# Performance work log

Hardware: AMD Instinct MI355X
Metric: run time of the kernel (lower is better)

Reference implementation:

```python
import jax, jax.numpy as jnp
import numpy as np


def setup_inputs() -> dict:
    key = jax.random.key(0)
    ks = jax.random.split(key, 9)
    B, L, Dh, Din = 8, 2048, 256, 1024  # Dh = hidden_size = input_dim // num_heads
    s = 0.05
    return {
        "x": jax.random.normal(ks[0], (B, L, Dh), dtype=jnp.float32),
        "Wq": jax.random.normal(ks[1], (Dh, Dh), dtype=jnp.float32) * s,
        "bq": jax.random.normal(ks[2], (Dh,), dtype=jnp.float32) * s,
        "Wk": jax.random.normal(ks[3], (Dh, Dh), dtype=jnp.float32) * s,
        "bk": jax.random.normal(ks[4], (Dh,), dtype=jnp.float32) * s,
        "Wv": jax.random.normal(ks[5], (Dh, Dh), dtype=jnp.float32) * s,
        "bv": jax.random.normal(ks[6], (Dh,), dtype=jnp.float32) * s,
        "Wo": jax.random.normal(ks[7], (Dh, Din), dtype=jnp.float32) * s,
        "bo": jax.random.normal(ks[8], (Din,), dtype=jnp.float32) * s,
        "num_heads": 4,
    }


def reference(x, Wq, bq, Wk, bk, Wv, bv, Wo, bo, num_heads):
    B, L, d = x.shape  # d == hidden_size; scale uses this full dim per the source
    H = num_heads
    hd = d // H
    # QKV projections (weights stored [in, out])
    Q = (x @ Wq + bq).reshape(B, L, H, hd).transpose(0, 2, 1, 3)  # [B,H,L,hd]
    K = (x @ Wk + bk).reshape(B, L, H, hd).transpose(0, 2, 1, 3)
    V = (x @ Wv + bv).reshape(B, L, H, hd).transpose(0, 2, 1, 3)
    scale = 1.0 / jnp.sqrt(jnp.float32(d))  # source divides by dim**0.5 with dim = x.shape[-1]
    scores = jnp.einsum("bhqd,bhkd->bhqk", Q, K) * scale  # [B,H,L,L]
    weights = jax.nn.softmax(scores, axis=-1)
    # dropout is identity in eval mode
    ctx = jnp.einsum("bhqk,bhkd->bhqd", weights, V)  # [B,H,L,hd]
    ctx = ctx.transpose(0, 2, 1, 3).reshape(B, L, d)
    return ctx @ Wo + bo  # [B,L,input_dim]
```

## Files before the change

kernel.cpp:

```cpp
#include <hip/hip_runtime.h>

#define SEQ   2048
#define NH    4
#define HD    64
#define DH    256
#define DIN   1024
#define MTOK  16384
#define BH    32

typedef _Float16 half8 __attribute__((ext_vector_type(8)));
typedef _Float16 half4 __attribute__((ext_vector_type(4)));
typedef float    floatx4 __attribute__((ext_vector_type(4)));

__device__ __forceinline__ floatx4 mfma16(half8 a, half8 b, floatx4 c) {
    return __builtin_amdgcn_mfma_f32_16x16x32_f16(a, b, c, 0, 0, 0);
}

#if __has_builtin(__builtin_amdgcn_exp2f)
#define EXP2(x) __builtin_amdgcn_exp2f(x)
#else
#define EXP2(x) exp2f(x)
#endif

__device__ __forceinline__ int swz(int r, int g) {
    return r * 64 + ((g ^ (r & 7)) << 3);
}

__device__ __forceinline__ void glds16(const _Float16* g, _Float16* l) {
    __builtin_amdgcn_global_load_lds(
        (const __attribute__((address_space(1))) void*)g,
        (__attribute__((address_space(3))) void*)l, 16, 0, 0);
}

#define QSCALE 0.09016844005556021f

__global__ __launch_bounds__(256) void cvt_kernel(
    const float* __restrict__ x, const float* __restrict__ Wq,
    const float* __restrict__ Wk, const float* __restrict__ Wv,
    const float* __restrict__ Wo, _Float16* __restrict__ xh,
    _Float16* __restrict__ Wtq, _Float16* __restrict__ WoT)
{
    const int t = threadIdx.x;
    if (blockIdx.x < 2048) {
        const size_t i = ((size_t)blockIdx.x * 256 + t) * 8;
        const float4 f0 = *(const float4*)(x + i);
        const float4 f1 = *(const float4*)(x + i + 4);
        half8 h;
        h[0]=(_Float16)f0.x; h[1]=(_Float16)f0.y; h[2]=(_Float16)f0.z; h[3]=(_Float16)f0.w;
        h[4]=(_Float16)f1.x; h[5]=(_Float16)f1.y; h[6]=(_Float16)f1.z; h[7]=(_Float16)f1.w;
        *(half8*)(xh + i) = h;
        return;
    }
    const int wb = blockIdx.x - 2048;
    const int nb = (wb % 28) * 64;
    const int kb = (wb / 28) * 64;
    const float* src; int ld, nc0;
    _Float16* dstbase; int nrow0;
    if (nb < 768) {
        src = (nb < 256) ? Wq : (nb < 512) ? Wk : Wv;
        ld = DH; nc0 = nb & 255; dstbase = Wtq; nrow0 = nb;
    } else { src = Wo; ld = DIN; nc0 = nb - 768; dstbase = WoT; nrow0 = nb - 768; }

    __shared__ float Ts[64][65];
    const int c = t & 63, r0 = t >> 6;
#pragma unroll
    for (int rr = 0; rr < 16; rr++)
        Ts[r0 + rr * 4][c] = src[(size_t)(kb + r0 + rr * 4) * ld + nc0 + c];
    __syncthreads();
    const int nr = t >> 2, kc = (t & 3) * 16;
    _Float16 hv[16];
#pragma unroll
    for (int j = 0; j < 16; j++) hv[j] = (_Float16)Ts[kc + j][nr];
    *(half8*)&dstbase[(size_t)(nrow0 + nr) * 256 + kb + kc]     = *(half8*)&hv[0];
    *(half8*)&dstbase[(size_t)(nrow0 + nr) * 256 + kb + kc + 8] = *(half8*)&hv[8];
}

__global__ __launch_bounds__(256) void qkv_kernel(
    const _Float16* __restrict__ xh, const _Float16* __restrict__ Wtq,
    const float* __restrict__ bq, const float* __restrict__ bk,
    const float* __restrict__ bv,
    _Float16* __restrict__ Qo, _Float16* __restrict__ Ko, _Float16* __restrict__ Vt)
{
    const int mb = blockIdx.x * 128;
    const int nb = blockIdx.y * 128;
    const int t = threadIdx.x, lane = t & 63, w = t >> 6;
    const int quad = lane >> 4, l16 = lane & 15;
    const int wr = (w >> 1) * 64, wc = (w & 1) * 64;
    const int which = nb >> 8;

    __shared__ _Float16 Ah[128 * 64];
    __shared__ _Float16 Bh[128 * 64];

    floatx4 acc[4][4] = {};

    const int srow = w * 8 + (lane >> 3);
    const int slg  = (lane & 7) ^ ((lane >> 3) & 7);
    const int sbase = w * 64;

    for (int k0 = 0; k0 < DH; k0 += 64) {
        __syncthreads();
#pragma unroll
        for (int c = 0; c < 4; c++) {
            glds16(xh + (size_t)(mb + c * 32 + srow) * DH + k0 + slg * 8,
                   &Ah[(c * 256 + sbase) * 8]);
            glds16(Wtq + (size_t)(nb + c * 32 + srow) * DH + k0 + slg * 8,
                   &Bh[(c * 256 + sbase) * 8]);
        }
        __syncthreads();
#pragma unroll
        for (int kh = 0; kh < 2; kh++) {
            half8 af[4], bf[4];
#pragma unroll
            for (int i = 0; i < 4; i++) {
                af[i] = *(const half8*)&Ah[swz(wr + i * 16 + l16, kh * 4 + quad)];
                bf[i] = *(const half8*)&Bh[swz(wc + i * 16 + l16, kh * 4 + quad)];
            }
            if (which == 2) {
#pragma unroll
                for (int mt = 0; mt < 4; mt++)
#pragma unroll
                    for (int nt = 0; nt < 4; nt++)
                        acc[mt][nt] = mfma16(af[mt], bf[nt], acc[mt][nt]);
            } else {
#pragma unroll
                for (int mt = 0; mt < 4; mt++)
#pragma unroll
                    for (int nt = 0; nt < 4; nt++)
                        acc[mt][nt] = mfma16(bf[nt], af[mt], acc[mt][nt]);
            }
        }
    }

    if (which == 2) {
#pragma unroll
        for (int nt = 0; nt < 4; nt++) {
            const int c2 = (nb & 255) + wc + nt * 16 + l16;
            const float bb = bv[c2];
            const int h = c2 >> 6, hd = c2 & 63;
#pragma unroll
            for (int mt = 0; mt < 4; mt++) {
                const int mr0 = mb + wr + mt * 16 + quad * 4;
                const int b = mr0 >> 11, lt0 = mr0 & (SEQ - 1);
                const int bh = b * NH + h;
                half4 hv;
#pragma unroll
                for (int i = 0; i < 4; i++) hv[i] = (_Float16)(acc[mt][nt][i] + bb);
                *(half4*)&Vt[((size_t)bh * HD + hd) * SEQ + lt0] = hv;
            }
        }
    } else {
        const float* bias = (which == 0) ? bq : bk;
        const float qs = (which == 0) ? QSCALE : 1.0f;
        _Float16* Out = (which == 0) ? Qo : Ko;
#pragma unroll
        for (int nt = 0; nt < 4; nt++) {
            const int c2b = (nb & 255) + wc + nt * 16 + quad * 4;
            const float4 bb4 = *(const float4*)&bias[c2b];
            const int h = c2b >> 6, hd0 = c2b & 63;
#pragma unroll
            for (int mt = 0; mt < 4; mt++) {
                const int tok = mb + wr + mt * 16 + l16;
                const int b = tok >> 11, lt = tok & (SEQ - 1);
                const int bh = b * NH + h;
                half4 hv;
                hv[0] = (_Float16)((acc[mt][nt][0] + bb4.x) * qs);
                hv[1] = (_Float16)((acc[mt][nt][1] + bb4.y) * qs);
                hv[2] = (_Float16)((acc[mt][nt][2] + bb4.z) * qs);
                hv[3] = (_Float16)((acc[mt][nt][3] + bb4.w) * qs);
                *(half4*)&Out[((size_t)bh * SEQ + lt) * HD + hd0] = hv;
            }
        }
    }
}

__global__ __launch_bounds__(256, 4) void attn_kernel(
    const _Float16* __restrict__ Q, const _Float16* __restrict__ K,
    const _Float16* __restrict__ Vt, _Float16* __restrict__ Opart,
    float* __restrict__ Lsum, int kspan)
{
    const int bh = blockIdx.y, qb = blockIdx.x * 128, ks = blockIdx.z;
    const int t = threadIdx.x, lane = t & 63, w = t >> 6;
    const int quad = lane >> 4, l16 = lane & 15;

    __shared__ _Float16 Ksm[64 * 64];
    __shared__ _Float16 Vsm[64 * 64];
    __shared__ _Float16 Psm[4 * 32 * 64];

    const _Float16* Kbh = K + (size_t)bh * SEQ * HD;
    const _Float16* Vbh = Vt + (size_t)bh * HD * SEQ;

    half8 qf[2][2];
#pragma unroll
    for (int qt = 0; qt < 2; qt++) {
        const _Float16* qp = Q + ((size_t)bh * SEQ + qb + w * 32 + qt * 16 + l16) * HD;
        qf[qt][0] = *(const half8*)(qp + quad * 8);
        qf[qt][1] = *(const half8*)(qp + 32 + quad * 8);
    }

    floatx4 oacc[2][4] = {};
    float lsum[2] = {0.f, 0.f};

    const int srow = w * 8 + (lane >> 3);
    const int slg  = (lane & 7) ^ ((lane >> 3) & 7);
    const int sbase = w * 64;
    const int pbase = w * 2048;
    const int kb0 = ks * kspan, kb1 = kb0 + kspan;

    for (int kb = kb0; kb < kb1; kb += 64) {
        __syncthreads();
#pragma unroll
        for (int c = 0; c < 2; c++) {
            glds16(Kbh + (size_t)(kb + c * 32 + srow) * HD + slg * 8,
                   &Ksm[(c * 256 + sbase) * 8]);
            glds16(Vbh + (size_t)(c * 32 + srow) * SEQ + kb + slg * 8,
                   &Vsm[(c * 256 + sbase) * 8]);
        }
        __syncthreads();

#pragma unroll
        for (int kt = 0; kt < 4; kt++) {
            const half8 kf0 = *(const half8*)&Ksm[swz(kt * 16 + l16, quad)];
            const half8 kf1 = *(const half8*)&Ksm[swz(kt * 16 + l16, 4 + quad)];
#pragma unroll
            for (int qt = 0; qt < 2; qt++) {
                floatx4 a = {};
                a = mfma16(kf0, qf[qt][0], a);
                a = mfma16(kf1, qf[qt][1], a);
                const float p0 = EXP2(a[0]), p1 = EXP2(a[1]);
                const float p2 = EXP2(a[2]), p3 = EXP2(a[3]);
                lsum[qt] += (p0 + p1) + (p2 + p3);
                half4 hp;
                hp[0] = (_Float16)p0; hp[1] = (_Float16)p1;
                hp[2] = (_Float16)p2; hp[3] = (_Float16)p3;
                const int g = kt * 2 + (quad >> 1);
                *(half4*)&Psm[pbase + (qt * 16 + l16) * 64 +
                              ((g ^ (l16 & 7)) << 3) + (quad & 1) * 4] = hp;
            }
        }

#pragma unroll
        for (int k2 = 0; k2 < 2; k2++) {
            half8 pf[2];
#pragma unroll
            for (int qt = 0; qt < 2; qt++)
                pf[qt] = *(const half8*)&Psm[pbase + swz(qt * 16 + l16, k2 * 4 + quad)];
#pragma unroll
            for (int nt = 0; nt < 4; nt++) {
                const half8 vf = *(const half8*)&Vsm[swz(nt * 16 + l16, k2 * 4 + quad)];
#pragma unroll
                for (int qt = 0; qt < 2; qt++)
                    oacc[qt][nt] = mfma16(vf, pf[qt], oacc[qt][nt]);
            }
        }
    }

#pragma unroll
    for (int qt = 0; qt < 2; qt++) {
        lsum[qt] += __shfl_xor(lsum[qt], 16, 64);
        lsum[qt] += __shfl_xor(lsum[qt], 32, 64);
        if (quad == 0)
            Lsum[((size_t)(ks * BH + bh)) * SEQ + qb + w * 32 + qt * 16 + l16] = lsum[qt];
    }
    _Float16* op = Opart + (((size_t)(ks * BH + bh)) * SEQ + qb + w * 32) * HD;
#pragma unroll
    for (int qt = 0; qt < 2; qt++)
#pragma unroll
        for (int nt = 0; nt < 4; nt++) {
            half4 hv;
#pragma unroll
            for (int i = 0; i < 4; i++) hv[i] = (_Float16)oacc[qt][nt][i];
            *(half4*)&op[(size_t)(qt * 16 + l16) * HD + nt * 16 + quad * 4] = hv;
        }
}

__global__ __launch_bounds__(256) void reduce_kernel(
    const _Float16* __restrict__ Opart, const float* __restrict__ Lsum,
    _Float16* __restrict__ ctx, int nks)
{
    const size_t i = ((size_t)blockIdx.x * 256 + threadIdx.x) * 8;
    const int ch = (int)(i & 255);
    const int h = ch >> 6, hd = ch & 63;
    const int tok = (int)(i >> 8);
    const int b = tok >> 11, l = tok & (SEQ - 1);
    const int bh = b * NH + h;

    float a[8] = {};
    float lt = 0.f;
    for (int ks = 0; ks < nks; ks++) {
        const size_t row = ((size_t)(ks * BH + bh)) * SEQ + l;
        lt += Lsum[row];
        const half8 v = *(const half8*)(Opart + row * HD + hd);
#pragma unroll
        for (int j = 0; j < 8; j++) a[j] += (float)v[j];
    }
    const float inv = 1.0f / lt;
    half8 o;
#pragma unroll
    for (int j = 0; j < 8; j++) o[j] = (_Float16)(a[j] * inv);
    *(half8*)(ctx + i) = o;
}

__global__ __launch_bounds__(256) void out_kernel(
    const _Float16* __restrict__ ctx, const _Float16* __restrict__ WoT,
    const float* __restrict__ bo, float* __restrict__ out)
{
    const int mb = blockIdx.x * 128;
    const int nb = blockIdx.y * 128;
    const int t = threadIdx.x, lane = t & 63, w = t >> 6;
    const int quad = lane >> 4, l16 = lane & 15;
    const int wr = (w >> 1) * 64, wc = (w & 1) * 64;

    __shared__ _Float16 Ah[128 * 64];
    __shared__ _Float16 Bh[128 * 64];

    floatx4 acc[4][4] = {};

    const int srow = w * 8 + (lane >> 3);
    const int slg  = (lane & 7) ^ ((lane >> 3) & 7);
    const int sbase = w * 64;

    for (int k0 = 0; k0 < DH; k0 += 64) {
        __syncthreads();
#pragma unroll
        for (int c = 0; c < 4; c++) {
            glds16(ctx + (size_t)(mb + c * 32 + srow) * DH + k0 + slg * 8,
                   &Ah[(c * 256 + sbase) * 8]);
            glds16(WoT + (size_t)(nb + c * 32 + srow) * DH + k0 + slg * 8,
                   &Bh[(c * 256 + sbase) * 8]);
        }
        __syncthreads();
#pragma unroll
        for (int kh = 0; kh < 2; kh++) {
            half8 af[4], bf[4];
#pragma unroll
            for (int i = 0; i < 4; i++) {
                af[i] = *(const half8*)&Ah[swz(wr + i * 16 + l16, kh * 4 + quad)];
                bf[i] = *(const half8*)&Bh[swz(wc + i * 16 + l16, kh * 4 + quad)];
            }
#pragma unroll
            for (int mt = 0; mt < 4; mt++)
#pragma unroll
                for (int nt = 0; nt < 4; nt++)
                    acc[mt][nt] = mfma16(bf[nt], af[mt], acc[mt][nt]);
        }
    }

#pragma unroll
    for (int nt = 0; nt < 4; nt++) {
        const int col0 = nb + wc + nt * 16 + quad * 4;
        const float4 bb4 = *(const float4*)&bo[col0];
#pragma unroll
        for (int mt = 0; mt < 4; mt++) {
            const int tok = mb + wr + mt * 16 + l16;
            float4 ov;
            ov.x = acc[mt][nt][0] + bb4.x;
            ov.y = acc[mt][nt][1] + bb4.y;
            ov.z = acc[mt][nt][2] + bb4.z;
            ov.w = acc[mt][nt][3] + bb4.w;
            *(float4*)&out[(size_t)tok * DIN + col0] = ov;
        }
    }
}

extern "C" void kernel_launch(void* const* d_in, const int* in_sizes, int n_in,
                              void* d_out, int out_size, void* d_ws, size_t ws_size,
                              hipStream_t stream) {
    (void)in_sizes; (void)n_in; (void)out_size;
    const float* x  = (const float*)d_in[0];
    const float* Wq = (const float*)d_in[1];
    const float* bq = (const float*)d_in[2];
    const float* Wk = (const float*)d_in[3];
    const float* bk = (const float*)d_in[4];
    const float* Wv = (const float*)d_in[5];
    const float* bv = (const float*)d_in[6];
    const float* Wo = (const float*)d_in[7];
    const float* bo = (const float*)d_in[8];

    const size_t H = (size_t)BH * SEQ * HD;
    _Float16* Qw  = (_Float16*)d_ws;
    _Float16* Kw  = Qw + H;
    _Float16* Vt  = Kw + H;
    _Float16* WoT = Vt + H;
    const size_t lsum_off = 3 * H + 262144;

    const size_t need4 = lsum_off * 2 + (size_t)4 * 65536 * 4 + (size_t)4 * H * 2;
    const int KS = (ws_size >= need4) ? 4 : 2;

    float* Lsum = (float*)(Qw + lsum_off);
    _Float16* Opart = Qw + lsum_off + (size_t)KS * 131072;
    _Float16* xh  = Opart;
    _Float16* Wtq = Opart + (size_t)MTOK * DH;
    _Float16* ctx = Qw;

    cvt_kernel<<<dim3(2048 + 112), 256, 0, stream>>>(x, Wq, Wk, Wv, Wo, xh, Wtq, WoT);
    qkv_kernel<<<dim3(MTOK / 128, 768 / 128), 256, 0, stream>>>(
        xh, Wtq, bq, bk, bv, Qw, Kw, Vt);
    attn_kernel<<<dim3(SEQ / 128, BH, KS), 256, 0, stream>>>(
        Qw, Kw, Vt, Opart, Lsum, SEQ / KS);
    reduce_kernel<<<dim3(MTOK * DH / (256 * 8)), 256, 0, stream>>>(
        Opart, Lsum, ctx, KS);
    out_kernel<<<dim3(MTOK / 128, DIN / 128), 256, 0, stream>>>(
        ctx, WoT, bo, (float*)d_out);
}
```

Measured before the change: 194.7 us.

## Load K/V fragments directly from global into registers, drop LDS staging in attention

The attention kernel stops staging K and V tiles through shared memory with barriers. Each wave now loads its MFMA fragments for K and V straight from global memory into registers, relying on L2/cache reuse across waves. The workspace is reorganised, the key-split count drops from 4/2 to 2/1, and occupancy is lowered to 3 blocks per CU. This removes the barriers and LDS traffic, but each of the four waves now issues its own redundant global loads for the same K/V data, and there are fewer key splits available for parallelism.

```diff
diff --git a/kernel.cpp b/kernel.cpp
--- a/kernel.cpp
+++ b/kernel.cpp
@@ -38,7 +38,7 @@
     const float* __restrict__ x, const float* __restrict__ Wq,
     const float* __restrict__ Wk, const float* __restrict__ Wv,
     const float* __restrict__ Wo, _Float16* __restrict__ xh,
-    _Float16* __restrict__ Wtq, _Float16* __restrict__ WoT)
+    _Float16* __restrict__ Wt)
 {
     const int t = threadIdx.x;
     if (blockIdx.x < 2048) {
@@ -55,11 +55,10 @@
     const int nb = (wb % 28) * 64;
     const int kb = (wb / 28) * 64;
     const float* src; int ld, nc0;
-    _Float16* dstbase; int nrow0;
     if (nb < 768) {
         src = (nb < 256) ? Wq : (nb < 512) ? Wk : Wv;
-        ld = DH; nc0 = nb & 255; dstbase = Wtq; nrow0 = nb;
-    } else { src = Wo; ld = DIN; nc0 = nb - 768; dstbase = WoT; nrow0 = nb - 768; }
+        ld = DH; nc0 = nb & 255;
+    } else { src = Wo; ld = DIN; nc0 = nb - 768; }
 
     __shared__ float Ts[64][65];
     const int c = t & 63, r0 = t >> 6;
@@ -71,12 +70,12 @@
     _Float16 hv[16];
 #pragma unroll
     for (int j = 0; j < 16; j++) hv[j] = (_Float16)Ts[kc + j][nr];
-    *(half8*)&dstbase[(size_t)(nrow0 + nr) * 256 + kb + kc]     = *(half8*)&hv[0];
-    *(half8*)&dstbase[(size_t)(nrow0 + nr) * 256 + kb + kc + 8] = *(half8*)&hv[8];
+    *(half8*)&Wt[(size_t)(nb + nr) * 256 + kb + kc]     = *(half8*)&hv[0];
+    *(half8*)&Wt[(size_t)(nb + nr) * 256 + kb + kc + 8] = *(half8*)&hv[8];
 }
 
 __global__ __launch_bounds__(256) void qkv_kernel(
-    const _Float16* __restrict__ xh, const _Float16* __restrict__ Wtq,
+    const _Float16* __restrict__ xh, const _Float16* __restrict__ Wt,
     const float* __restrict__ bq, const float* __restrict__ bk,
     const float* __restrict__ bv,
     _Float16* __restrict__ Qo, _Float16* __restrict__ Ko, _Float16* __restrict__ Vt)
@@ -103,7 +102,7 @@
         for (int c = 0; c < 4; c++) {
             glds16(xh + (size_t)(mb + c * 32 + srow) * DH + k0 + slg * 8,
                    &Ah[(c * 256 + sbase) * 8]);
-            glds16(Wtq + (size_t)(nb + c * 32 + srow) * DH + k0 + slg * 8,
+            glds16(Wt + (size_t)(nb + c * 32 + srow) * DH + k0 + slg * 8,
                    &Bh[(c * 256 + sbase) * 8]);
         }
         __syncthreads();
@@ -173,7 +172,7 @@
     }
 }
 
-__global__ __launch_bounds__(256, 4) void attn_kernel(
+__global__ __launch_bounds__(256, 3) void attn_kernel(
     const _Float16* __restrict__ Q, const _Float16* __restrict__ K,
     const _Float16* __restrict__ Vt, _Float16* __restrict__ Opart,
     float* __restrict__ Lsum, int kspan)
@@ -182,12 +181,9 @@
     const int t = threadIdx.x, lane = t & 63, w = t >> 6;
     const int quad = lane >> 4, l16 = lane & 15;
 
-    __shared__ _Float16 Ksm[64 * 64];
-    __shared__ _Float16 Vsm[64 * 64];
     __shared__ _Float16 Psm[4 * 32 * 64];
 
-    const _Float16* Kbh = K + (size_t)bh * SEQ * HD;
-    const _Float16* Vbh = Vt + (size_t)bh * HD * SEQ;
+    const int kb0 = ks * kspan;
 
     half8 qf[2][2];
 #pragma unroll
@@ -200,32 +196,32 @@
     floatx4 oacc[2][4] = {};
     float lsum[2] = {0.f, 0.f};
 
-    const int srow = w * 8 + (lane >> 3);
-    const int slg  = (lane & 7) ^ ((lane >> 3) & 7);
-    const int sbase = w * 64;
+    const _Float16* kp = K + ((size_t)bh * SEQ + kb0 + l16) * HD + quad * 8;
+    const _Float16* vp = Vt + ((size_t)bh * HD + l16) * SEQ + kb0 + quad * 8;
+
     const int pbase = w * 2048;
-    const int kb0 = ks * kspan, kb1 = kb0 + kspan;
-
-    for (int kb = kb0; kb < kb1; kb += 64) {
-        __syncthreads();
-#pragma unroll
-        for (int c = 0; c < 2; c++) {
-            glds16(Kbh + (size_t)(kb + c * 32 + srow) * HD + slg * 8,
-                   &Ksm[(c * 256 + sbase) * 8]);
-            glds16(Vbh + (size_t)(c * 32 + srow) * SEQ + kb + slg * 8,
-                   &Vsm[(c * 256 + sbase) * 8]);
-        }
-        __syncthreads();
-
+
+    for (int kb = 0; kb < kspan; kb += 64) {
+        half8 kf0[4], kf1[4];
 #pragma unroll
         for (int kt = 0; kt < 4; kt++) {
-            const half8 kf0 = *(const half8*)&Ksm[swz(kt * 16 + l16, quad)];
-            const half8 kf1 = *(const half8*)&Ksm[swz(kt * 16 + l16, 4 + quad)];
+            kf0[kt] = *(const half8*)(kp + kt * 16 * HD);
+            kf1[kt] = *(const half8*)(kp + kt * 16 * HD + 32);
+        }
+        half8 vf[2][4];
+#pragma unroll
+        for (int nt = 0; nt < 4; nt++) {
+            vf[0][nt] = *(const half8*)(vp + (size_t)nt * 16 * SEQ);
+            vf[1][nt] = *(const half8*)(vp + (size_t)nt * 16 * SEQ + 32);
+        }
+
+#pragma unroll
+        for (int kt = 0; kt < 4; kt++) {
 #pragma unroll
             for (int qt = 0; qt < 2; qt++) {
                 floatx4 a = {};
-                a = mfma16(kf0, qf[qt][0], a);
-                a = mfma16(kf1, qf[qt][1], a);
+                a = mfma16(kf0[kt], qf[qt][0], a);
+                a = mfma16(kf1[kt], qf[qt][1], a);
                 const float p0 = EXP2(a[0]), p1 = EXP2(a[1]);
                 const float p2 = EXP2(a[2]), p3 = EXP2(a[3]);
                 lsum[qt] += (p0 + p1) + (p2 + p3);
@@ -245,13 +241,14 @@
             for (int qt = 0; qt < 2; qt++)
                 pf[qt] = *(const half8*)&Psm[pbase + swz(qt * 16 + l16, k2 * 4 + quad)];
 #pragma unroll
-            for (int nt = 0; nt < 4; nt++) {
-                const half8 vf = *(const half8*)&Vsm[swz(nt * 16 + l16, k2 * 4 + quad)];
+            for (int nt = 0; nt < 4; nt++)
 #pragma unroll
                 for (int qt = 0; qt < 2; qt++)
-                    oacc[qt][nt] = mfma16(vf, pf[qt], oacc[qt][nt]);
-            }
-        }
+                    oacc[qt][nt] = mfma16(vf[k2][nt], pf[qt], oacc[qt][nt]);
+        }
+
+        kp += 64 * HD;
+        vp += 64;
     }
 
 #pragma unroll
@@ -377,28 +374,26 @@
     const float* bo = (const float*)d_in[8];
 
     const size_t H = (size_t)BH * SEQ * HD;
-    _Float16* Qw  = (_Float16*)d_ws;
-    _Float16* Kw  = Qw + H;
-    _Float16* Vt  = Kw + H;
-    _Float16* WoT = Vt + H;
-    const size_t lsum_off = 3 * H + 262144;
-
-    const size_t need4 = lsum_off * 2 + (size_t)4 * 65536 * 4 + (size_t)4 * H * 2;
-    const int KS = (ws_size >= need4) ? 4 : 2;
-
-    float* Lsum = (float*)(Qw + lsum_off);
-    _Float16* Opart = Qw + lsum_off + (size_t)KS * 131072;
-    _Float16* xh  = Opart;
-    _Float16* Wtq = Opart + (size_t)MTOK * DH;
-    _Float16* ctx = Qw;
-
-    cvt_kernel<<<dim3(2048 + 112), 256, 0, stream>>>(x, Wq, Wk, Wv, Wo, xh, Wtq, WoT);
+    _Float16* Qw = (_Float16*)d_ws;
+    _Float16* Kw = Qw + H;
+    _Float16* Vt = Kw + H;
+    _Float16* xh = Vt + H;
+    _Float16* Wt = xh + (size_t)MTOK * DH;
+    _Float16* Opart = Wt + (size_t)1792 * 256;
+
+    const size_t base_bytes = (3 * H + (size_t)MTOK * DH + (size_t)1792 * 256) * 2;
+    const size_t per_ks = H * 2 + (size_t)BH * SEQ * 4;
+    const int KS = (ws_size >= base_bytes + 2 * per_ks) ? 2 : 1;
+    float* Lsum = (float*)(Opart + (size_t)KS * H);
+    _Float16* ctx = xh;
+
+    cvt_kernel<<<dim3(2048 + 112), 256, 0, stream>>>(x, Wq, Wk, Wv, Wo, xh, Wt);
     qkv_kernel<<<dim3(MTOK / 128, 768 / 128), 256, 0, stream>>>(
-        xh, Wtq, bq, bk, bv, Qw, Kw, Vt);
+        xh, Wt, bq, bk, bv, Qw, Kw, Vt);
     attn_kernel<<<dim3(SEQ / 128, BH, KS), 256, 0, stream>>>(
         Qw, Kw, Vt, Opart, Lsum, SEQ / KS);
     reduce_kernel<<<dim3(MTOK * DH / (256 * 8)), 256, 0, stream>>>(
         Opart, Lsum, ctx, KS);
     out_kernel<<<dim3(MTOK / 128, DIN / 128), 256, 0, stream>>>(
-        ctx, WoT, bo, (float*)d_out);
-}
+        ctx, Wt + (size_t)768 * DH, bo, (float*)d_out);
+}
```

Result: slower. 268.6 us (+38.0%).
